# Performance work log

Measured on AMD Instinct MI355X. Metric: run time of the kernel, lower is better.

The kernel has to match this reference:

```python
import jax, jax.numpy as jnp
import numpy as np

B, C, H, W = 8, 256, 128, 128
HEADS, DIM_HEAD = 4, 32
HID = HEADS * DIM_HEAD  # 128


def setup_inputs() -> dict:
    key = jax.random.key(0)
    k1, k2, k3, k4 = jax.random.split(key, 4)
    x = jax.random.normal(k1, (B, C, H, W), dtype=jnp.float32)
    # 1x1 conv weights stored as [out_ch, in_ch]
    w_qkv = jax.random.normal(k2, (3 * HID, C), dtype=jnp.float32) * (1.0 / np.sqrt(C))
    w_out = jax.random.normal(k3, (C, HID), dtype=jnp.float32) * (1.0 / np.sqrt(HID))
    b_out = jax.random.normal(k4, (C,), dtype=jnp.float32) * 0.01
    return {"x": x, "w_qkv": w_qkv, "w_out": w_out, "b_out": b_out}


def reference(x, w_qkv, w_out, b_out):
    b, c, h, w = x.shape
    n = h * w
    # 1x1 conv == channel matmul
    qkv = jnp.einsum('oc,bchw->bohw', w_qkv, x)  # [b, 3*HID, h, w]
    q, k, v = jnp.split(qkv, 3, axis=1)
    # rearrange 'b (heads d) h w -> b heads d (h w)'
    def to_heads(t):
        return t.reshape(b, HEADS, DIM_HEAD, n)
    q, k, v = to_heads(q), to_heads(k), to_heads(v)
    k = jax.nn.softmax(k, axis=-1)  # over spatial n
    # q_scale is False: q used as-is
    context = jnp.einsum('bhdn,bhen->bhde', k, v)   # [b, heads, d, e] small
    out = jnp.einsum('bhde,bhdn->bhen', context, q)  # [b, heads, e, n]
    out = out.reshape(b, HID, h, w)
    out = jnp.einsum('oc,bchw->bohw', w_out, out) + b_out[None, :, None, None]
    return out
```

## Files before the change

kernel.cpp:

```cpp
#include <hip/hip_runtime.h>
#include <stdint.h>

#define BB 8
#define CIN 256
#define NSP 16384
#define HID 128

typedef __bf16 bfrag __attribute__((ext_vector_type(8)));
typedef float  f32x4 __attribute__((ext_vector_type(4)));

__device__ __forceinline__ unsigned short f2bf(float f) {
  union { float f; unsigned int u; } v; v.f = f;
  unsigned int u = v.u;
  return (unsigned short)((u + 0x7FFFu + ((u >> 16) & 1u)) >> 16);
}

__global__ __launch_bounds__(512, 4) void la_fused(const float* __restrict__ x,
                                                   const float* __restrict__ w_qkv,
                                                   float* __restrict__ ctxp,
                                                   float* __restrict__ sums) {
  __shared__ __align__(16) union {
    struct { unsigned short Wt[256][40]; unsigned short Xb[128][40]; } g;
    struct { unsigned short Lk[64][136]; unsigned short Lv[64][136];
             float Pc[4][1024]; } e;
  } sh;
  const int chunk = blockIdx.x;
  const int n0 = chunk * 128;
  const int b = blockIdx.y;
  const int t = threadIdx.x;
  const int lane = t & 63, wv = t >> 6;
  const int l15 = lane & 15, q = lane >> 4;
  const int cl = t & 31;
  const int n16 = (t >> 5) * 8;
  const float* xp = x + (size_t)b * CIN * NSP + n0;
  const float* wkv = w_qkv + (size_t)128 * CIN;
  f32x4 acc[2][8];
#pragma unroll
  for (int i = 0; i < 2; ++i)
#pragma unroll
    for (int j = 0; j < 8; ++j) acc[i][j] = 0.0f;

  float4 xa0, xa1;
  {
    const float* xr = xp + (size_t)cl * NSP + n16;
    xa0 = *(const float4*)xr;
    xa1 = *(const float4*)(xr + 4);
  }

  for (int kc = 0; kc < 8; ++kc) {
    sh.g.Xb[n16 + 0][cl] = f2bf(xa0.x);
    sh.g.Xb[n16 + 1][cl] = f2bf(xa0.y);
    sh.g.Xb[n16 + 2][cl] = f2bf(xa0.z);
    sh.g.Xb[n16 + 3][cl] = f2bf(xa0.w);
    sh.g.Xb[n16 + 4][cl] = f2bf(xa1.x);
    sh.g.Xb[n16 + 5][cl] = f2bf(xa1.y);
    sh.g.Xb[n16 + 6][cl] = f2bf(xa1.z);
    sh.g.Xb[n16 + 7][cl] = f2bf(xa1.w);
#pragma unroll
    for (int i = 0; i < 2; ++i) {
      const int id = t + i * 512;
      const int row = id >> 2, c8 = (id & 3) * 8;
      const float* wr = wkv + (size_t)row * CIN + kc * 32 + c8;
      const float4 wa = *(const float4*)wr;
      const float4 wb4 = *(const float4*)(wr + 4);
      ushort4 p0, p1;
      p0.x = f2bf(wa.x); p0.y = f2bf(wa.y); p0.z = f2bf(wa.z); p0.w = f2bf(wa.w);
      p1.x = f2bf(wb4.x); p1.y = f2bf(wb4.y); p1.z = f2bf(wb4.z); p1.w = f2bf(wb4.w);
      *(ushort4*)&sh.g.Wt[row][c8] = p0;
      *(ushort4*)&sh.g.Wt[row][c8 + 4] = p1;
    }
    __syncthreads();
    if (kc < 7) {
      const float* xr = xp + (size_t)((kc + 1) * 32 + cl) * NSP + n16;
      xa0 = *(const float4*)xr;
      xa1 = *(const float4*)(xr + 4);
    }
    bfrag a0 = *(const bfrag*)&sh.g.Wt[wv * 16 + l15][q * 8];
    bfrag a1 = *(const bfrag*)&sh.g.Wt[128 + wv * 16 + l15][q * 8];
#pragma unroll
    for (int ni = 0; ni < 8; ++ni) {
      bfrag bbv = *(const bfrag*)&sh.g.Xb[ni * 16 + l15][q * 8];
      acc[0][ni] = __builtin_amdgcn_mfma_f32_16x16x32_bf16(a0, bbv, acc[0][ni], 0, 0, 0);
      acc[1][ni] = __builtin_amdgcn_mfma_f32_16x16x32_bf16(a1, bbv, acc[1][ni], 0, 0, 0);
    }
    __syncthreads();
  }

#pragma unroll
  for (int ni = 0; ni < 8; ++ni)
#pragma unroll
    for (int rg = 0; rg < 4; ++rg) acc[0][ni][rg] = __expf(acc[0][ni][rg]);

  {
    float sp[4] = {0.f, 0.f, 0.f, 0.f};
#pragma unroll
    for (int ni = 0; ni < 8; ++ni)
#pragma unroll
      for (int rg = 0; rg < 4; ++rg) sp[rg] += acc[0][ni][rg];
#pragma unroll
    for (int rg = 0; rg < 4; ++rg) {
      float s = sp[rg];
      s += __shfl_down(s, 8, 16);
      s += __shfl_down(s, 4, 16);
      s += __shfl_down(s, 2, 16);
      s += __shfl_down(s, 1, 16);
      if (l15 == 0) atomicAdd(&sums[b * 128 + wv * 16 + q * 4 + rg], s);
    }
  }
  float* cp = ctxp + ((size_t)chunk * 32 + b * 4) * 1024;
#pragma unroll
  for (int ph = 0; ph < 2; ++ph) {
    if ((wv >> 2) == ph) {
      const int r = (wv & 3) * 16 + q * 4;
#pragma unroll
      for (int ni = 0; ni < 8; ++ni)
#pragma unroll
        for (int rg = 0; rg < 4; ++rg) {
          sh.e.Lk[r + rg][ni * 16 + l15] = f2bf(acc[0][ni][rg]);
          sh.e.Lv[r + rg][ni * 16 + l15] = f2bf(acc[1][ni][rg]);
        }
    }
    __syncthreads();
    const int hl = wv >> 2, nq = wv & 3;
    f32x4 c2[2][2];
    c2[0][0] = 0.f; c2[0][1] = 0.f; c2[1][0] = 0.f; c2[1][1] = 0.f;
    bfrag ka[2], vb[2];
#pragma unroll
    for (int d2 = 0; d2 < 2; ++d2)
      ka[d2] = *(const bfrag*)&sh.e.Lk[hl * 32 + d2 * 16 + l15][nq * 32 + q * 8];
#pragma unroll
    for (int e2 = 0; e2 < 2; ++e2)
      vb[e2] = *(const bfrag*)&sh.e.Lv[hl * 32 + e2 * 16 + l15][nq * 32 + q * 8];
#pragma unroll
    for (int d2 = 0; d2 < 2; ++d2)
#pragma unroll
      for (int e2 = 0; e2 < 2; ++e2)
        c2[d2][e2] = __builtin_amdgcn_mfma_f32_16x16x32_bf16(ka[d2], vb[e2], c2[d2][e2], 0, 0, 0);
    const int slot = hl * 2 + (nq & 1);
    if (nq < 2) {
#pragma unroll
      for (int d2 = 0; d2 < 2; ++d2)
#pragma unroll
        for (int e2 = 0; e2 < 2; ++e2)
#pragma unroll
          for (int rg = 0; rg < 4; ++rg)
            sh.e.Pc[slot][(d2 * 16 + q * 4 + rg) * 32 + e2 * 16 + l15] = c2[d2][e2][rg];
    }
    __syncthreads();
    if (nq >= 2) {
#pragma unroll
      for (int d2 = 0; d2 < 2; ++d2)
#pragma unroll
        for (int e2 = 0; e2 < 2; ++e2)
#pragma unroll
          for (int rg = 0; rg < 4; ++rg)
            sh.e.Pc[slot][(d2 * 16 + q * 4 + rg) * 32 + e2 * 16 + l15] += c2[d2][e2][rg];
    }
    __syncthreads();
    for (int idx = t; idx < 2048; idx += 512) {
      const int h2 = idx >> 10, pos = idx & 1023;
      cp[(ph * 2 + h2) * 1024 + pos] = sh.e.Pc[h2 * 2][pos] + sh.e.Pc[h2 * 2 + 1][pos];
    }
    __syncthreads();
  }
}

__global__ __launch_bounds__(256) void la_reduce(const float* __restrict__ ctxp,
                                                 float* __restrict__ ctxu) {
  const int gid = blockIdx.x * 256 + threadIdx.x;
  float s = 0.f;
#pragma unroll 8
  for (int c = 0; c < 128; ++c) s += ctxp[(size_t)c * 32768 + gid];
  ctxu[gid] = s;
}

__global__ __launch_bounds__(128) void la_weff(const float* __restrict__ w_out,
                                               const float* __restrict__ ctxu,
                                               const float* __restrict__ sums,
                                               float* __restrict__ weffF) {
  const int o = blockIdx.x;
  const int b = blockIdx.y;
  const int cp = threadIdx.x;
  const int h = cp >> 5, d = cp & 31;
  const float* wrow = w_out + (size_t)o * HID + h * 32;
  const float* crow = ctxu + ((size_t)(b * 4 + h) * 32 + d) * 32;
  float s = 0.f;
#pragma unroll 8
  for (int e = 0; e < 32; ++e) s += wrow[e] * crow[e];
  s *= (1.0f / sums[b * 128 + h * 32 + d]);
  weffF[((size_t)b * 256 + o) * HID + cp] = s;
}

__global__ __launch_bounds__(256) void la_wcomb(const float* __restrict__ weffF,
                                                const float* __restrict__ w_qkv,
                                                unsigned short* __restrict__ wcomb) {
  __shared__ float ws[128];
  const int o = blockIdx.x;
  const int b = blockIdx.y;
  const int t = threadIdx.x;
  if (t < 128) ws[t] = weffF[((size_t)b * 256 + o) * HID + t];
  __syncthreads();
  float s = 0.f;
#pragma unroll 8
  for (int hd = 0; hd < 128; ++hd) s += ws[hd] * w_qkv[(size_t)hd * CIN + t];
  wcomb[((size_t)b * 256 + o) * 256 + t] = f2bf(s);
}

__global__ __launch_bounds__(512, 4) void la_out(const unsigned short* __restrict__ wcomb,
                                                 const float* __restrict__ x,
                                                 const float* __restrict__ b_out,
                                                 float* __restrict__ out) {
  __shared__ __align__(16) unsigned short At[256][40];
  __shared__ __align__(16) unsigned short Bt[128][40];
  const int n0 = blockIdx.x * 128;
  const int b = blockIdx.y;
  const int t = threadIdx.x;
  const int lane = t & 63, wv = t >> 6;
  const int l15 = lane & 15, q = lane >> 4;
  const int wm = (wv & 3) * 64;
  const int wn = (wv >> 2) * 64;
  const int cl = t & 31, n16 = (t >> 5) * 8;
  const float* xp = x + (size_t)b * CIN * NSP + n0;
  const unsigned short* abase = wcomb + (size_t)b * 256 * 256;
  f32x4 acc[4][4];
#pragma unroll
  for (int i = 0; i < 4; ++i)
#pragma unroll
    for (int j = 0; j < 4; ++j) acc[i][j] = 0.0f;

  float4 xa0, xa1;
  {
    const float* xr = xp + (size_t)cl * NSP + n16;
    xa0 = *(const float4*)xr;
    xa1 = *(const float4*)(xr + 4);
  }

  for (int kc = 0; kc < 8; ++kc) {
    Bt[n16 + 0][cl] = f2bf(xa0.x);
    Bt[n16 + 1][cl] = f2bf(xa0.y);
    Bt[n16 + 2][cl] = f2bf(xa0.z);
    Bt[n16 + 3][cl] = f2bf(xa0.w);
    Bt[n16 + 4][cl] = f2bf(xa1.x);
    Bt[n16 + 5][cl] = f2bf(xa1.y);
    Bt[n16 + 6][cl] = f2bf(xa1.z);
    Bt[n16 + 7][cl] = f2bf(xa1.w);
#pragma unroll
    for (int i = 0; i < 2; ++i) {
      const int id = t + i * 512;
      const int row = id >> 2, c8 = (id & 3) * 8;
      *(uint4*)&At[row][c8] = *(const uint4*)(abase + (size_t)row * 256 + kc * 32 + c8);
    }
    __syncthreads();
    if (kc < 7) {
      const float* xr = xp + (size_t)((kc + 1) * 32 + cl) * NSP + n16;
      xa0 = *(const float4*)xr;
      xa1 = *(const float4*)(xr + 4);
    }
    bfrag a[4];
#pragma unroll
    for (int mi = 0; mi < 4; ++mi) a[mi] = *(const bfrag*)&At[wm + mi * 16 + l15][q * 8];
#pragma unroll
    for (int ni = 0; ni < 4; ++ni) {
      bfrag bbv = *(const bfrag*)&Bt[wn + ni * 16 + l15][q * 8];
#pragma unroll
      for (int mi = 0; mi < 4; ++mi)
        acc[mi][ni] = __builtin_amdgcn_mfma_f32_16x16x32_bf16(a[mi], bbv, acc[mi][ni], 0, 0, 0);
    }
    __syncthreads();
  }
  float* obase = out + (size_t)b * 256 * NSP;
#pragma unroll
  for (int mi = 0; mi < 4; ++mi) {
    const int ob = wm + mi * 16 + q * 4;
    const float4 bias = *(const float4*)(b_out + ob);
    float ba[4] = {bias.x, bias.y, bias.z, bias.w};
#pragma unroll
    for (int ni = 0; ni < 4; ++ni) {
      const int n = n0 + wn + ni * 16 + l15;
#pragma unroll
      for (int rg = 0; rg < 4; ++rg)
        obase[(size_t)(ob + rg) * NSP + n] = acc[mi][ni][rg] + ba[rg];
    }
  }
}


extern "C" void kernel_launch(void* const* d_in, const int* in_sizes, int n_in,
                              void* d_out, int out_size, void* d_ws, size_t ws_size,
                              hipStream_t stream) {
  (void)in_sizes; (void)n_in; (void)out_size; (void)ws_size;
  const float* x     = (const float*)d_in[0];
  const float* w_qkv = (const float*)d_in[1];
  const float* w_out = (const float*)d_in[2];
  const float* b_out = (const float*)d_in[3];
  float* out = (float*)d_out;
  char* ws = (char*)d_ws;
  float* ctxp          = (float*)(ws);
  float* ctxu          = (float*)(ws + 16777216);
  float* sums          = (float*)(ws + 16908288);
  float* weffF         = (float*)(ws + 16912384);
  unsigned short* wcomb = (unsigned short*)(ws + 17960960);

  hipMemsetAsync(sums, 0, 4096, stream);
  la_fused<<<dim3(NSP / 128, BB), dim3(512), 0, stream>>>(x, w_qkv, ctxp, sums);
  la_reduce<<<dim3(128), dim3(256), 0, stream>>>(ctxp, ctxu);
  la_weff<<<dim3(256, BB), dim3(128), 0, stream>>>(w_out, ctxu, sums, weffF);
  la_wcomb<<<dim3(256, BB), dim3(256), 0, stream>>>(weffF, w_qkv, wcomb);
  la_out<<<dim3(NSP / 128, BB), dim3(512), 0, stream>>>(wcomb, x, b_out, out);
}
```

Baseline: 346.6 us.

## Double-buffer X tiles, read bf16 weights from global, fuse reduce/weff/wcomb kernels

A prep kernel now converts the k/v weights to bf16 once and zeroes the context and sum buffers, which replaces the memset. Both GEMM kernels read the A operand straight from global/L2 instead of staging it in LDS, and double-buffer the X tile in shared memory. That removes one barrier per k-step and lets the next chunk's stores overlap the MFMAs. Partial contexts are atomically accumulated into ctxu, so the separate reduce kernel and the 16MB partial buffer go away, and the weff and wcomb kernels are merged into one. The trade-offs are more global-load latency for the A fragments and atomic contention on ctxu.

```diff
diff --git a/kernel.cpp b/kernel.cpp
--- a/kernel.cpp
+++ b/kernel.cpp
@@ -15,12 +15,31 @@
   return (unsigned short)((u + 0x7FFFu + ((u >> 16) & 1u)) >> 16);
 }
 
+__global__ __launch_bounds__(256) void la_prep(const float* __restrict__ w_qkv,
+                                               unsigned short* __restrict__ wkvb,
+                                               float* __restrict__ zbase) {
+  const int blk = blockIdx.x;
+  const int t = threadIdx.x;
+  if (blk < 64) {
+    const int off = (blk * 256 + t) * 4;
+    const float4 wv4 = *(const float4*)(w_qkv + (size_t)128 * CIN + off);
+    ushort4 p;
+    p.x = f2bf(wv4.x); p.y = f2bf(wv4.y); p.z = f2bf(wv4.z); p.w = f2bf(wv4.w);
+    *(ushort4*)(wkvb + off) = p;
+  } else {
+    for (int i = t; i < 8448; i += 256) {
+      float4 z = {0.f, 0.f, 0.f, 0.f};
+      *(float4*)(zbase + i * 4) = z;
+    }
+  }
+}
+
 __global__ __launch_bounds__(512, 4) void la_fused(const float* __restrict__ x,
-                                                   const float* __restrict__ w_qkv,
-                                                   float* __restrict__ ctxp,
+                                                   const unsigned short* __restrict__ wkvb,
+                                                   float* __restrict__ ctxu,
                                                    float* __restrict__ sums) {
   __shared__ __align__(16) union {
-    struct { unsigned short Wt[256][40]; unsigned short Xb[128][40]; } g;
+    struct { unsigned short Xb[2][128][40]; } g;
     struct { unsigned short Lk[64][136]; unsigned short Lv[64][136];
              float Pc[4][1024]; } e;
   } sh;
@@ -33,7 +52,6 @@
   const int cl = t & 31;
   const int n16 = (t >> 5) * 8;
   const float* xp = x + (size_t)b * CIN * NSP + n0;
-  const float* wkv = w_qkv + (size_t)128 * CIN;
   f32x4 acc[2][8];
 #pragma unroll
   for (int i = 0; i < 2; ++i)
@@ -46,40 +64,44 @@
     xa0 = *(const float4*)xr;
     xa1 = *(const float4*)(xr + 4);
   }
-
+  {
+    sh.g.Xb[0][n16 + 0][cl] = f2bf(xa0.x);
+    sh.g.Xb[0][n16 + 1][cl] = f2bf(xa0.y);
+    sh.g.Xb[0][n16 + 2][cl] = f2bf(xa0.z);
+    sh.g.Xb[0][n16 + 3][cl] = f2bf(xa0.w);
+    sh.g.Xb[0][n16 + 4][cl] = f2bf(xa1.x);
+    sh.g.Xb[0][n16 + 5][cl] = f2bf(xa1.y);
+    sh.g.Xb[0][n16 + 6][cl] = f2bf(xa1.z);
+    sh.g.Xb[0][n16 + 7][cl] = f2bf(xa1.w);
+    const float* xr = xp + (size_t)(32 + cl) * NSP + n16;
+    xa0 = *(const float4*)xr;
+    xa1 = *(const float4*)(xr + 4);
+  }
+  __syncthreads();
+
+#pragma unroll
   for (int kc = 0; kc < 8; ++kc) {
-    sh.g.Xb[n16 + 0][cl] = f2bf(xa0.x);
-    sh.g.Xb[n16 + 1][cl] = f2bf(xa0.y);
-    sh.g.Xb[n16 + 2][cl] = f2bf(xa0.z);
-    sh.g.Xb[n16 + 3][cl] = f2bf(xa0.w);
-    sh.g.Xb[n16 + 4][cl] = f2bf(xa1.x);
-    sh.g.Xb[n16 + 5][cl] = f2bf(xa1.y);
-    sh.g.Xb[n16 + 6][cl] = f2bf(xa1.z);
-    sh.g.Xb[n16 + 7][cl] = f2bf(xa1.w);
-#pragma unroll
-    for (int i = 0; i < 2; ++i) {
-      const int id = t + i * 512;
-      const int row = id >> 2, c8 = (id & 3) * 8;
-      const float* wr = wkv + (size_t)row * CIN + kc * 32 + c8;
-      const float4 wa = *(const float4*)wr;
-      const float4 wb4 = *(const float4*)(wr + 4);
-      ushort4 p0, p1;
-      p0.x = f2bf(wa.x); p0.y = f2bf(wa.y); p0.z = f2bf(wa.z); p0.w = f2bf(wa.w);
-      p1.x = f2bf(wb4.x); p1.y = f2bf(wb4.y); p1.z = f2bf(wb4.z); p1.w = f2bf(wb4.w);
-      *(ushort4*)&sh.g.Wt[row][c8] = p0;
-      *(ushort4*)&sh.g.Wt[row][c8 + 4] = p1;
-    }
-    __syncthreads();
+    const int p = kc & 1;
+    bfrag a0 = *(const bfrag*)(wkvb + (size_t)(wv * 16 + l15) * CIN + kc * 32 + q * 8);
+    bfrag a1 = *(const bfrag*)(wkvb + (size_t)(128 + wv * 16 + l15) * CIN + kc * 32 + q * 8);
     if (kc < 7) {
-      const float* xr = xp + (size_t)((kc + 1) * 32 + cl) * NSP + n16;
-      xa0 = *(const float4*)xr;
-      xa1 = *(const float4*)(xr + 4);
-    }
-    bfrag a0 = *(const bfrag*)&sh.g.Wt[wv * 16 + l15][q * 8];
-    bfrag a1 = *(const bfrag*)&sh.g.Wt[128 + wv * 16 + l15][q * 8];
+      sh.g.Xb[p ^ 1][n16 + 0][cl] = f2bf(xa0.x);
+      sh.g.Xb[p ^ 1][n16 + 1][cl] = f2bf(xa0.y);
+      sh.g.Xb[p ^ 1][n16 + 2][cl] = f2bf(xa0.z);
+      sh.g.Xb[p ^ 1][n16 + 3][cl] = f2bf(xa0.w);
+      sh.g.Xb[p ^ 1][n16 + 4][cl] = f2bf(xa1.x);
+      sh.g.Xb[p ^ 1][n16 + 5][cl] = f2bf(xa1.y);
+      sh.g.Xb[p ^ 1][n16 + 6][cl] = f2bf(xa1.z);
+      sh.g.Xb[p ^ 1][n16 + 7][cl] = f2bf(xa1.w);
+      if (kc < 6) {
+        const float* xr = xp + (size_t)((kc + 2) * 32 + cl) * NSP + n16;
+        xa0 = *(const float4*)xr;
+        xa1 = *(const float4*)(xr + 4);
+      }
+    }
 #pragma unroll
     for (int ni = 0; ni < 8; ++ni) {
-      bfrag bbv = *(const bfrag*)&sh.g.Xb[ni * 16 + l15][q * 8];
+      bfrag bbv = *(const bfrag*)&sh.g.Xb[p][ni * 16 + l15][q * 8];
       acc[0][ni] = __builtin_amdgcn_mfma_f32_16x16x32_bf16(a0, bbv, acc[0][ni], 0, 0, 0);
       acc[1][ni] = __builtin_amdgcn_mfma_f32_16x16x32_bf16(a1, bbv, acc[1][ni], 0, 0, 0);
     }
@@ -107,7 +129,6 @@
       if (l15 == 0) atomicAdd(&sums[b * 128 + wv * 16 + q * 4 + rg], s);
     }
   }
-  float* cp = ctxp + ((size_t)chunk * 32 + b * 4) * 1024;
 #pragma unroll
   for (int ph = 0; ph < 2; ++ph) {
     if ((wv >> 2) == ph) {
@@ -159,50 +180,35 @@
     __syncthreads();
     for (int idx = t; idx < 2048; idx += 512) {
       const int h2 = idx >> 10, pos = idx & 1023;
-      cp[(ph * 2 + h2) * 1024 + pos] = sh.e.Pc[h2 * 2][pos] + sh.e.Pc[h2 * 2 + 1][pos];
-    }
-    __syncthreads();
-  }
-}
-
-__global__ __launch_bounds__(256) void la_reduce(const float* __restrict__ ctxp,
-                                                 float* __restrict__ ctxu) {
-  const int gid = blockIdx.x * 256 + threadIdx.x;
-  float s = 0.f;
-#pragma unroll 8
-  for (int c = 0; c < 128; ++c) s += ctxp[(size_t)c * 32768 + gid];
-  ctxu[gid] = s;
-}
-
-__global__ __launch_bounds__(128) void la_weff(const float* __restrict__ w_out,
-                                               const float* __restrict__ ctxu,
-                                               const float* __restrict__ sums,
-                                               float* __restrict__ weffF) {
-  const int o = blockIdx.x;
-  const int b = blockIdx.y;
-  const int cp = threadIdx.x;
-  const int h = cp >> 5, d = cp & 31;
-  const float* wrow = w_out + (size_t)o * HID + h * 32;
-  const float* crow = ctxu + ((size_t)(b * 4 + h) * 32 + d) * 32;
-  float s = 0.f;
-#pragma unroll 8
-  for (int e = 0; e < 32; ++e) s += wrow[e] * crow[e];
-  s *= (1.0f / sums[b * 128 + h * 32 + d]);
-  weffF[((size_t)b * 256 + o) * HID + cp] = s;
-}
-
-__global__ __launch_bounds__(256) void la_wcomb(const float* __restrict__ weffF,
-                                                const float* __restrict__ w_qkv,
-                                                unsigned short* __restrict__ wcomb) {
-  __shared__ float ws[128];
+      atomicAdd(&ctxu[(size_t)b * 4096 + (ph * 2 + h2) * 1024 + pos],
+                sh.e.Pc[h2 * 2][pos] + sh.e.Pc[h2 * 2 + 1][pos]);
+    }
+    __syncthreads();
+  }
+}
+
+__global__ __launch_bounds__(256) void la_mid(const float* __restrict__ w_out,
+                                              const float* __restrict__ ctxu,
+                                              const float* __restrict__ sums,
+                                              const float* __restrict__ w_qkv,
+                                              unsigned short* __restrict__ wcomb) {
+  __shared__ float wrow[128];
   const int o = blockIdx.x;
   const int b = blockIdx.y;
   const int t = threadIdx.x;
-  if (t < 128) ws[t] = weffF[((size_t)b * 256 + o) * HID + t];
+  if (t < 128) {
+    const int h = t >> 5, d = t & 31;
+    const float* wr = w_out + (size_t)o * HID + h * 32;
+    const float* cr = ctxu + ((size_t)(b * 4 + h) * 32 + d) * 32;
+    float s = 0.f;
+#pragma unroll 8
+    for (int e = 0; e < 32; ++e) s += wr[e] * cr[e];
+    wrow[t] = s * (1.0f / sums[b * 128 + t]);
+  }
   __syncthreads();
   float s = 0.f;
 #pragma unroll 8
-  for (int hd = 0; hd < 128; ++hd) s += ws[hd] * w_qkv[(size_t)hd * CIN + t];
+  for (int hd = 0; hd < 128; ++hd) s += wrow[hd] * w_qkv[(size_t)hd * CIN + t];
   wcomb[((size_t)b * 256 + o) * 256 + t] = f2bf(s);
 }
 
@@ -210,8 +216,7 @@
                                                  const float* __restrict__ x,
                                                  const float* __restrict__ b_out,
                                                  float* __restrict__ out) {
-  __shared__ __align__(16) unsigned short At[256][40];
-  __shared__ __align__(16) unsigned short Bt[128][40];
+  __shared__ __align__(16) unsigned short Bt[2][128][40];
   const int n0 = blockIdx.x * 128;
   const int b = blockIdx.y;
   const int t = threadIdx.x;
@@ -234,34 +239,46 @@
     xa0 = *(const float4*)xr;
     xa1 = *(const float4*)(xr + 4);
   }
-
+  {
+    Bt[0][n16 + 0][cl] = f2bf(xa0.x);
+    Bt[0][n16 + 1][cl] = f2bf(xa0.y);
+    Bt[0][n16 + 2][cl] = f2bf(xa0.z);
+    Bt[0][n16 + 3][cl] = f2bf(xa0.w);
+    Bt[0][n16 + 4][cl] = f2bf(xa1.x);
+    Bt[0][n16 + 5][cl] = f2bf(xa1.y);
+    Bt[0][n16 + 6][cl] = f2bf(xa1.z);
+    Bt[0][n16 + 7][cl] = f2bf(xa1.w);
+    const float* xr = xp + (size_t)(32 + cl) * NSP + n16;
+    xa0 = *(const float4*)xr;
+    xa1 = *(const float4*)(xr + 4);
+  }
+  __syncthreads();
+
+#pragma unroll
   for (int kc = 0; kc < 8; ++kc) {
-    Bt[n16 + 0][cl] = f2bf(xa0.x);
-    Bt[n16 + 1][cl] = f2bf(xa0.y);
-    Bt[n16 + 2][cl] = f2bf(xa0.z);
-    Bt[n16 + 3][cl] = f2bf(xa0.w);
-    Bt[n16 + 4][cl] = f2bf(xa1.x);
-    Bt[n16 + 5][cl] = f2bf(xa1.y);
-    Bt[n16 + 6][cl] = f2bf(xa1.z);
-    Bt[n16 + 7][cl] = f2bf(xa1.w);
-#pragma unroll
-    for (int i = 0; i < 2; ++i) {
-      const int id = t + i * 512;
-      const int row = id >> 2, c8 = (id & 3) * 8;
-      *(uint4*)&At[row][c8] = *(const uint4*)(abase + (size_t)row * 256 + kc * 32 + c8);
-    }
-    __syncthreads();
+    const int p = kc & 1;
+    bfrag a[4];
+#pragma unroll
+    for (int mi = 0; mi < 4; ++mi)
+      a[mi] = *(const bfrag*)(abase + (size_t)(wm + mi * 16 + l15) * 256 + kc * 32 + q * 8);
     if (kc < 7) {
-      const float* xr = xp + (size_t)((kc + 1) * 32 + cl) * NSP + n16;
-      xa0 = *(const float4*)xr;
-      xa1 = *(const float4*)(xr + 4);
-    }
-    bfrag a[4];
-#pragma unroll
-    for (int mi = 0; mi < 4; ++mi) a[mi] = *(const bfrag*)&At[wm + mi * 16 + l15][q * 8];
+      Bt[p ^ 1][n16 + 0][cl] = f2bf(xa0.x);
+      Bt[p ^ 1][n16 + 1][cl] = f2bf(xa0.y);
+      Bt[p ^ 1][n16 + 2][cl] = f2bf(xa0.z);
+      Bt[p ^ 1][n16 + 3][cl] = f2bf(xa0.w);
+      Bt[p ^ 1][n16 + 4][cl] = f2bf(xa1.x);
+      Bt[p ^ 1][n16 + 5][cl] = f2bf(xa1.y);
+      Bt[p ^ 1][n16 + 6][cl] = f2bf(xa1.z);
+      Bt[p ^ 1][n16 + 7][cl] = f2bf(xa1.w);
+      if (kc < 6) {
+        const float* xr = xp + (size_t)((kc + 2) * 32 + cl) * NSP + n16;
+        xa0 = *(const float4*)xr;
+        xa1 = *(const float4*)(xr + 4);
+      }
+    }
 #pragma unroll
     for (int ni = 0; ni < 4; ++ni) {
-      bfrag bbv = *(const bfrag*)&Bt[wn + ni * 16 + l15][q * 8];
+      bfrag bbv = *(const bfrag*)&Bt[p][wn + ni * 16 + l15][q * 8];
 #pragma unroll
       for (int mi = 0; mi < 4; ++mi)
         acc[mi][ni] = __builtin_amdgcn_mfma_f32_16x16x32_bf16(a[mi], bbv, acc[mi][ni], 0, 0, 0);
@@ -295,16 +312,13 @@
   const float* b_out = (const float*)d_in[3];
   float* out = (float*)d_out;
   char* ws = (char*)d_ws;
-  float* ctxp          = (float*)(ws);
-  float* ctxu          = (float*)(ws + 16777216);
-  float* sums          = (float*)(ws + 16908288);
-  float* weffF         = (float*)(ws + 16912384);
-  unsigned short* wcomb = (unsigned short*)(ws + 17960960);
-
-  hipMemsetAsync(sums, 0, 4096, stream);
-  la_fused<<<dim3(NSP / 128, BB), dim3(512), 0, stream>>>(x, w_qkv, ctxp, sums);
-  la_reduce<<<dim3(128), dim3(256), 0, stream>>>(ctxp, ctxu);
-  la_weff<<<dim3(256, BB), dim3(128), 0, stream>>>(w_out, ctxu, sums, weffF);
-  la_wcomb<<<dim3(256, BB), dim3(256), 0, stream>>>(weffF, w_qkv, wcomb);
+  unsigned short* wkvb  = (unsigned short*)(ws);
+  float* ctxu           = (float*)(ws + 131072);
+  float* sums           = (float*)(ws + 262144);
+  unsigned short* wcomb = (unsigned short*)(ws + 266240);
+
+  la_prep<<<dim3(65), dim3(256), 0, stream>>>(w_qkv, wkvb, ctxu);
+  la_fused<<<dim3(NSP / 128, BB), dim3(512), 0, stream>>>(x, wkvb, ctxu, sums);
+  la_mid<<<dim3(256, BB), dim3(256), 0, stream>>>(w_out, ctxu, sums, w_qkv, wcomb);
   la_out<<<dim3(NSP / 128, BB), dim3(512), 0, stream>>>(wcomb, x, b_out, out);
 }
```

Result: faster. 329.3 us (-5.0%).
